# Performance work log

Measured on AMD Instinct MI355X. Metric: run time of the kernel, lower is better.

The kernel has to match this reference:

```python
import jax, jax.numpy as jnp
import numpy as np

N_NODES = 10000
N_EDGES = 160000
HID = 256
NBOND = 6
NATOM = 62
NLAYERS = 6


def _lin_init(key, fan_in, fan_out):
    # torch nn.Linear default: U(-1/sqrt(fan_in), 1/sqrt(fan_in))
    kw, kb = jax.random.split(key)
    bound = 1.0 / np.sqrt(fan_in)
    w = jax.random.uniform(kw, (fan_in, fan_out), jnp.float32, -bound, bound)
    b = jax.random.uniform(kb, (fan_out,), jnp.float32, -bound, bound)
    return w, b


def setup_inputs() -> dict:
    key = jax.random.key(0)
    ks = jax.random.split(key, 32)
    atom_features = jax.random.normal(ks[0], (N_NODES, NATOM), jnp.float32)
    edge_index = jax.random.randint(ks[1], (2, N_EDGES), 0, N_NODES, jnp.int64 if jax.config.jax_enable_x64 else jnp.int32)
    edge_features = jax.random.normal(ks[2], (N_EDGES, NBOND), jnp.float32)

    embed_w, embed_b = _lin_init(ks[3], NATOM, HID)

    msg_in = 2 * HID + NBOND  # 518
    mw1, mb1, mw2, mb2 = [], [], [], []
    uw1, ub1, uw2, ub2 = [], [], [], []
    for i in range(NLAYERS):
        k = jax.random.split(ks[4 + i], 4)
        w, b = _lin_init(k[0], msg_in, HID); mw1.append(w); mb1.append(b)
        w, b = _lin_init(k[1], HID, HID); mw2.append(w); mb2.append(b)
        w, b = _lin_init(k[2], 2 * HID, HID); uw1.append(w); ub1.append(b)
        w, b = _lin_init(k[3], HID, HID); uw2.append(w); ub2.append(b)

    r_w1, r_b1 = _lin_init(ks[20], HID, HID)
    r_w2, r_b2 = _lin_init(ks[21], HID, HID // 2)
    r_w3, r_b3 = _lin_init(ks[22], HID // 2, 1)

    return {
        "atom_features": atom_features,
        "edge_index": edge_index,
        "edge_features": edge_features,
        "embed_w": embed_w, "embed_b": embed_b,
        "msg_w1": jnp.stack(mw1), "msg_b1": jnp.stack(mb1),
        "msg_w2": jnp.stack(mw2), "msg_b2": jnp.stack(mb2),
        "upd_w1": jnp.stack(uw1), "upd_b1": jnp.stack(ub1),
        "upd_w2": jnp.stack(uw2), "upd_b2": jnp.stack(ub2),
        "r_w1": r_w1, "r_b1": r_b1,
        "r_w2": r_w2, "r_b2": r_b2,
        "r_w3": r_w3, "r_b3": r_b3,
    }


def _mlp2(x, w1, b1, w2, b2):
    return jnp.maximum(x @ w1 + b1, 0.0) @ w2 + b2


def reference(atom_features, edge_index, edge_features,
              embed_w, embed_b,
              msg_w1, msg_b1, msg_w2, msg_b2,
              upd_w1, upd_b1, upd_w2, upd_b2,
              r_w1, r_b1, r_w2, r_b2, r_w3, r_b3):
    src, dst = edge_index[0], edge_index[1]
    n = atom_features.shape[0]
    x = atom_features @ embed_w + embed_b  # [N, H]
    for l in range(msg_w1.shape[0]):
        # per-edge gather + concat -> message MLP
        msg_in = jnp.concatenate([x[src], x[dst], edge_features], axis=-1)  # [E, 2H+B]
        msgs = _mlp2(msg_in, msg_w1[l], msg_b1[l], msg_w2[l], msg_b2[l])  # [E, H]
        # scatter-add into dst nodes
        agg = jax.ops.segment_sum(msgs, dst, num_segments=n)  # [N, H]
        x = _mlp2(jnp.concatenate([x, agg], axis=-1), upd_w1[l], upd_b1[l], upd_w2[l], upd_b2[l])
    # readout (dropout is identity in eval mode)
    h = jnp.maximum(x @ r_w1 + r_b1, 0.0)
    h = jnp.maximum(h @ r_w2 + r_b2, 0.0)
    out = h @ r_w3 + r_b3  # [N, 1]
    return out.mean(axis=0)  # [1]
```

## Files before the change

### kernel.cpp

```cpp
#include <hip/hip_runtime.h>
#include <hip/hip_bf16.h>
#include <hip/hip_fp16.h>


#define HID 256

typedef _Float16 h8 __attribute__((ext_vector_type(8)));
typedef float f32x4 __attribute__((ext_vector_type(4)));

__device__ __forceinline__ void unpack_h8(const int4& r, float* f) {
    const __half2* h = reinterpret_cast<const __half2*>(&r);
#pragma unroll
    for (int k = 0; k < 4; ++k) {
        float2 t = __half22float2(h[k]);
        f[2 * k] = t.x;
        f[2 * k + 1] = t.y;
    }
}

__device__ __forceinline__ void unpack_h4(const int2& r, float* f) {
    const __half2* h = reinterpret_cast<const __half2*>(&r);
    float2 t0 = __half22float2(h[0]);
    float2 t1 = __half22float2(h[1]);
    f[0] = t0.x; f[1] = t0.y; f[2] = t1.x; f[3] = t1.y;
}

__device__ __forceinline__ void gld16(const void* g, void* l) {
    __builtin_amdgcn_global_load_lds(
        (const __attribute__((address_space(1))) void*)g,
        (__attribute__((address_space(3))) void*)l, 16, 0, 0);
}

__device__ __forceinline__ int swz(int row) { return (row + (row >> 2)) & 3; }


__global__ void hist_act_kernel(const int* __restrict__ dst, int* __restrict__ deg,
                                int E, const float* __restrict__ atom,
                                __half* __restrict__ atomH, int NA) {
    int i = blockIdx.x * blockDim.x + threadIdx.x;
    if (i < E) atomicAdd(&deg[dst[i]], 1);
    if (i < NA) {
        int r = i >> 3, seg = i & 7;
        h8 v;
#pragma unroll
        for (int j = 0; j < 8; ++j) {
            int c = seg * 8 + j;
            v[j] = (_Float16)((c < 62) ? atom[(size_t)r * 62 + c] : 0.f);
        }
        *reinterpret_cast<h8*>(&atomH[(size_t)r * 64 + seg * 8]) = v;
    }
}

__global__ __launch_bounds__(256) void scan_kernel(
    const int* __restrict__ deg, int* __restrict__ offs, float* __restrict__ degf, int n) {
    __shared__ int ws[4];
    const int t = threadIdx.x;
    const int lane = t & 63;
    const int w = t >> 6;
    const int per = (n + 255) / 256;
    const int s = t * per;
    const int e = min(s + per, n);
    int sum = 0;
    for (int i = s; i < e; ++i) sum += deg[i];
    int v = sum;
#pragma unroll
    for (int off = 1; off < 64; off <<= 1) {
        int u = __shfl_up(v, off, 64);
        if (lane >= off) v += u;
    }
    if (lane == 63) ws[w] = v;
    __syncthreads();
    if (t == 0) {
        int c = 0;
#pragma unroll
        for (int i = 0; i < 4; ++i) { int x = ws[i]; ws[i] = c; c += x; }
    }
    __syncthreads();
    int run = ws[w] + v - sum;
    for (int i = s; i < e; ++i) {
        int d = deg[i];
        offs[i] = run;
        degf[i] = (float)d;
        run += d;
    }
    if (e == n) offs[n] = run;
}


struct CDesc {
    const float* src;
    __half* dst;
    int Kreal, Kpad, srcN, tile0;
};
struct CTab {
    CDesc d[32];
    int nd;
};

__device__ void convert_body(const CTab& tab, int bid) {
    int idx = 0;
    for (int i = 1; i < tab.nd; ++i)
        if (tab.d[i].tile0 <= bid) idx = i;
    const CDesc d = tab.d[idx];
    const int q = bid - d.tile0;
    const int ntN = d.srcN >> 6;
    const int kb = (q / ntN) * 32;
    const int nb = (q % ntN) * 64;
    const int n = nb + (threadIdx.x & 63);
    const int k0 = kb + (threadIdx.x >> 6) * 8;
    h8 v;
#pragma unroll
    for (int j = 0; j < 8; ++j) {
        int k = k0 + j;
        v[j] = (_Float16)((k < d.Kreal) ? d.src[(size_t)k * d.srcN + n] : 0.f);
    }
    *reinterpret_cast<h8*>(&d.dst[(size_t)n * d.Kpad + k0]) = v;
}

__global__ __launch_bounds__(256) void scatter_conv_kernel(
    const int* __restrict__ src, const int* __restrict__ dst,
    const int* __restrict__ offs, int* __restrict__ cursor,
    int* __restrict__ csr_src, const float* __restrict__ ef,
    __half* __restrict__ ef8, int E, int sblocks, CTab tab) {
    if ((int)blockIdx.x < sblocks) {
        int i = blockIdx.x * blockDim.x + threadIdx.x;
        if (i < E) {
            int d = dst[i];
            int pos = atomicAdd(&cursor[d], 1);
            int idx = offs[d] + pos;
            csr_src[idx] = src[i];
            const float* s6 = ef + (size_t)i * 6;
            unsigned short h[8];
#pragma unroll
            for (int j = 0; j < 6; ++j) h[j] = __half_as_ushort(__float2half_rn(s6[j]));
            h[6] = 0; h[7] = 0;
            int4 pk;
            pk.x = (int)(h[0] | ((unsigned)h[1] << 16));
            pk.y = (int)(h[2] | ((unsigned)h[3] << 16));
            pk.z = (int)(h[4] | ((unsigned)h[5] << 16));
            pk.w = (int)(h[6] | ((unsigned)h[7] << 16));
            *reinterpret_cast<int4*>(ef8 + (size_t)idx * 8) = pk;
        }
    } else {
        convert_body(tab, blockIdx.x - sblocks);
    }
}


struct BDesc { float* out; const float* base; const float* v1; const float* B1;
               const float* v2; const float* B2; };
struct BTab { BDesc d[31]; };


#define ASTR 40

struct FDesc { const float* U2; const __half* Wfb; __half* dst; };
struct FTab { FDesc d[22]; };

__global__ __launch_bounds__(256) void fold_bias_kernel(FTab tab, BTab bt, int fblocks) {
    if ((int)blockIdx.x >= fblocks) {
        const BDesc d = bt.d[blockIdx.x - fblocks];
        const int j = threadIdx.x;
        float acc = d.base ? d.base[j] : 0.f;
        if (d.v1)
            for (int k = 0; k < 256; ++k) acc = fmaf(d.v1[k], d.B1[(size_t)k * 256 + j], acc);
        if (d.v2)
            for (int k = 0; k < 256; ++k) acc = fmaf(d.v2[k], d.B2[(size_t)k * 256 + j], acc);
        d.out[j] = acc;
        return;
    }
    const FDesc dd = tab.d[blockIdx.x >> 4];
    const int t4 = blockIdx.x & 15;
    const int rowBase = (t4 >> 2) * 64;
    const int colBase = (t4 & 3) * 64;

    __shared__ __align__(16) _Float16 Ah[64 * ASTR];
    __shared__ __align__(16) _Float16 Bh[64 * ASTR];

    const int tid = threadIdx.x;
    const int lane = tid & 63;
    const int wave = tid >> 6;
    const int waveM = (wave >> 1) * 32;
    const int waveN = (wave & 1) * 32;
    const int m0 = lane & 15;
    const int quad = lane >> 4;
    const int sr = tid >> 2;
    const int sseg = tid & 3;

    const f32x4 z = {0.f, 0.f, 0.f, 0.f};
    f32x4 acc[2][2] = {{z, z}, {z, z}};

    for (int kb = 0; kb < 256; kb += 32) {
        {
            size_t off = (size_t)(rowBase + sr) * 256 + kb + sseg * 8;
            *reinterpret_cast<int4*>(&Ah[sr * ASTR + sseg * 8]) =
                *reinterpret_cast<const int4*>(&dd.Wfb[off]);
        }
        {
            const float* Bp = dd.U2 + (size_t)(colBase + sr) * 256 + kb + sseg * 8;
            float4 u0 = *reinterpret_cast<const float4*>(Bp);
            float4 u1 = *reinterpret_cast<const float4*>(Bp + 4);
            h8 v;
            v[0] = (_Float16)u0.x; v[1] = (_Float16)u0.y;
            v[2] = (_Float16)u0.z; v[3] = (_Float16)u0.w;
            v[4] = (_Float16)u1.x; v[5] = (_Float16)u1.y;
            v[6] = (_Float16)u1.z; v[7] = (_Float16)u1.w;
            *reinterpret_cast<h8*>(&Bh[sr * ASTR + sseg * 8]) = v;
        }
        __syncthreads();

        const h8 a0 = *reinterpret_cast<const h8*>(&Ah[(waveM + m0) * ASTR + quad * 8]);
        const h8 a1 = *reinterpret_cast<const h8*>(&Ah[(waveM + 16 + m0) * ASTR + quad * 8]);
        const h8 b0 = *reinterpret_cast<const h8*>(&Bh[(waveN + m0) * ASTR + quad * 8]);
        const h8 b1 = *reinterpret_cast<const h8*>(&Bh[(waveN + 16 + m0) * ASTR + quad * 8]);

        acc[0][0] = __builtin_amdgcn_mfma_f32_16x16x32_f16(a0, b0, acc[0][0], 0, 0, 0);
        acc[0][1] = __builtin_amdgcn_mfma_f32_16x16x32_f16(a0, b1, acc[0][1], 0, 0, 0);
        acc[1][0] = __builtin_amdgcn_mfma_f32_16x16x32_f16(a1, b0, acc[1][0], 0, 0, 0);
        acc[1][1] = __builtin_amdgcn_mfma_f32_16x16x32_f16(a1, b1, acc[1][1], 0, 0, 0);

        __syncthreads();
    }

#pragma unroll
    for (int tm = 0; tm < 2; ++tm)
#pragma unroll
        for (int reg = 0; reg < 4; ++reg) {
            int n = rowBase + waveM + tm * 16 + quad * 4 + reg;
#pragma unroll
            for (int tn = 0; tn < 2; ++tn) {
                int k = colBase + waveN + tn * 16 + m0;
                dd.dst[(size_t)n * 256 + k] = __float2half_rn(acc[tm][tn][reg]);
            }
        }
}


template <int TN>
__global__ __launch_bounds__(256) void mfma_gemm(
    const __half* __restrict__ A, int lda,
    const __half* __restrict__ W, int K,
    const float* __restrict__ bias, const float* __restrict__ bias2,
    const float* __restrict__ rowscale,
    const __half* __restrict__ addend, int astride,
    __half* __restrict__ C, int M, int Nc, int do_relu) {
    constexpr int BUF = 4096 + TN * 2048;
    __shared__ __align__(16) unsigned char lds[2 * BUF];

    const int tid = threadIdx.x;
    const int lane = tid & 63;
    const int wave = tid >> 6;
    const int m0 = lane & 15;
    const int quad = lane >> 4;
    const int waveM = (wave >> 1) * 32;
    const int waveN = (wave & 1) * (TN * 16);
    const int rowBase = blockIdx.x * 64;
    const int colBase = blockIdx.y * (TN * 32);

    const int sa_r = tid >> 2;
    const int sa_ks = (tid & 3) ^ swz(sa_r);
    const int sa_row = min(rowBase + sa_r, M - 1);
    const int sb_r1 = sa_r + 64;
    const int sb_ks1 = (tid & 3) ^ swz(sb_r1);

    int aoff[2], boff[TN];
#pragma unroll
    for (int tm = 0; tm < 2; ++tm) {
        int r = waveM + tm * 16 + m0;
        aoff[tm] = ((r << 2) + (quad ^ swz(r))) << 4;
    }
#pragma unroll
    for (int tn = 0; tn < TN; ++tn) {
        int r = waveN + tn * 16 + m0;
        boff[tn] = 4096 + (((r << 2) + (quad ^ swz(r))) << 4);
    }

    const f32x4 z = {0.f, 0.f, 0.f, 0.f};
    f32x4 acc[2][TN];
#pragma unroll
    for (int tm = 0; tm < 2; ++tm)
#pragma unroll
        for (int tn = 0; tn < TN; ++tn) acc[tm][tn] = z;

    const __half* ga = A + (size_t)sa_row * lda + sa_ks * 8;
    const __half* gb0 = W + (size_t)(colBase + sa_r) * K + sa_ks * 8;
    const __half* gb1 = W + (size_t)(colBase + sb_r1) * K + sb_ks1 * 8;

    auto issue = [&](int p, int kb) {
        unsigned char* base = lds + p * BUF;
        gld16(ga + kb, base + wave * 1024);
        gld16(gb0 + kb, base + 4096 + wave * 1024);
        if constexpr (TN == 4) gld16(gb1 + kb, base + 8192 + wave * 1024);
    };

    issue(0, 0);
    int p = 0;
    for (int kb = 0; kb < K; kb += 32) {
        const bool has_next = (kb + 32 < K);
        if (has_next) issue(p ^ 1, kb + 32);
        if (has_next) {
            if constexpr (TN == 4)
                asm volatile("s_waitcnt vmcnt(3)" ::: "memory");
            else
                asm volatile("s_waitcnt vmcnt(2)" ::: "memory");
        } else {
            asm volatile("s_waitcnt vmcnt(0)" ::: "memory");
        }
        asm volatile("s_barrier" ::: "memory");

        const unsigned char* base = lds + p * BUF;
        h8 ah[2], bh[TN];
#pragma unroll
        for (int tm = 0; tm < 2; ++tm)
            ah[tm] = *reinterpret_cast<const h8*>(base + aoff[tm]);
#pragma unroll
        for (int tn = 0; tn < TN; ++tn)
            bh[tn] = *reinterpret_cast<const h8*>(base + boff[tn]);
#pragma unroll
        for (int tm = 0; tm < 2; ++tm)
#pragma unroll
            for (int tn = 0; tn < TN; ++tn)
                acc[tm][tn] = __builtin_amdgcn_mfma_f32_16x16x32_f16(
                    ah[tm], bh[tn], acc[tm][tn], 0, 0, 0);
        asm volatile("s_waitcnt lgkmcnt(0)" ::: "memory");
        asm volatile("s_barrier" ::: "memory");
        p ^= 1;
    }

    float cb[TN], db[TN];
    int col[TN];
#pragma unroll
    for (int tn = 0; tn < TN; ++tn) {
        col[tn] = colBase + waveN + tn * 16 + m0;
        cb[tn] = bias ? bias[col[tn]] : 0.f;
        db[tn] = bias2 ? bias2[col[tn]] : 0.f;
    }
#pragma unroll
    for (int tm = 0; tm < 2; ++tm) {
#pragma unroll
        for (int reg = 0; reg < 4; ++reg) {
            int row = rowBase + waveM + tm * 16 + quad * 4 + reg;
            if (row >= M) continue;
            float rs = rowscale ? rowscale[row] : 0.0f;
#pragma unroll
            for (int tn = 0; tn < TN; ++tn) {
                float v = acc[tm][tn][reg] + cb[tn] + rs * db[tn];
                if (addend)
                    v += __half2float(addend[(size_t)row * astride + col[tn]]);
                if (do_relu) v = fmaxf(v, 0.f);
                C[(size_t)row * Nc + col[tn]] = __float2half_rn(v);
            }
        }
    }
}


__global__ __launch_bounds__(256) void aggregate_kernel(
    const __half* __restrict__ PQ, const __half* __restrict__ ef8,
    const int* __restrict__ offs, const int* __restrict__ csr_src,
    const float* __restrict__ W1c, __half* __restrict__ Hagg, int n) {
    const int wave = threadIdx.x >> 6;
    const int lane = threadIdx.x & 63;
    const int node = blockIdx.x * 4 + wave;
    if (node >= n) return;
    const int ch = lane * 4;

    float wc[6][4];
#pragma unroll
    for (int k = 0; k < 6; ++k) {
        float4 w0 = *reinterpret_cast<const float4*>(W1c + k * HID + ch);
        wc[k][0] = w0.x; wc[k][1] = w0.y; wc[k][2] = w0.z; wc[k][3] = w0.w;
    }
    float qb[4];
    unpack_h4(*reinterpret_cast<const int2*>(PQ + (size_t)node * 768 + 256 + ch), qb);

    float acc[4] = {0.f, 0.f, 0.f, 0.f};

    auto fma_edge = [&](const int2& praw, const int4& eraw) {
        float p[4], e[8];
        unpack_h4(praw, p);
        unpack_h8(eraw, e);
#pragma unroll
        for (int i = 0; i < 4; ++i) {
            float h = p[i] + qb[i];
            h = fmaf(e[0], wc[0][i], h);
            h = fmaf(e[1], wc[1][i], h);
            h = fmaf(e[2], wc[2][i], h);
            h = fmaf(e[3], wc[3][i], h);
            h = fmaf(e[4], wc[4][i], h);
            h = fmaf(e[5], wc[5][i], h);
            acc[i] += fmaxf(h, 0.f);
        }
    };

    const int beg = offs[node];
    const int end = offs[node + 1];
    int j = beg;

    while (j + 6 <= end) {
        int s0 = csr_src[j];
        int s1 = csr_src[j + 1];
        int s2 = csr_src[j + 2];
        int s3 = csr_src[j + 3];
        int s4 = csr_src[j + 4];
        int s5 = csr_src[j + 5];
        int4 e0 = *reinterpret_cast<const int4*>(ef8 + (size_t)j * 8);
        int4 e1 = *reinterpret_cast<const int4*>(ef8 + (size_t)(j + 1) * 8);
        int4 e2 = *reinterpret_cast<const int4*>(ef8 + (size_t)(j + 2) * 8);
        int4 e3 = *reinterpret_cast<const int4*>(ef8 + (size_t)(j + 3) * 8);
        int4 e4 = *reinterpret_cast<const int4*>(ef8 + (size_t)(j + 4) * 8);
        int4 e5 = *reinterpret_cast<const int4*>(ef8 + (size_t)(j + 5) * 8);
        int2 p0 = *reinterpret_cast<const int2*>(PQ + (size_t)s0 * 768 + ch);
        int2 p1 = *reinterpret_cast<const int2*>(PQ + (size_t)s1 * 768 + ch);
        int2 p2 = *reinterpret_cast<const int2*>(PQ + (size_t)s2 * 768 + ch);
        int2 p3 = *reinterpret_cast<const int2*>(PQ + (size_t)s3 * 768 + ch);
        int2 p4 = *reinterpret_cast<const int2*>(PQ + (size_t)s4 * 768 + ch);
        int2 p5 = *reinterpret_cast<const int2*>(PQ + (size_t)s5 * 768 + ch);
        fma_edge(p0, e0);
        fma_edge(p1, e1);
        fma_edge(p2, e2);
        fma_edge(p3, e3);
        fma_edge(p4, e4);
        fma_edge(p5, e5);
        j += 6;
    }
    while (j + 2 <= end) {
        int s0 = csr_src[j];
        int s1 = csr_src[j + 1];
        int4 e0 = *reinterpret_cast<const int4*>(ef8 + (size_t)j * 8);
        int4 e1 = *reinterpret_cast<const int4*>(ef8 + (size_t)(j + 1) * 8);
        int2 p0 = *reinterpret_cast<const int2*>(PQ + (size_t)s0 * 768 + ch);
        int2 p1 = *reinterpret_cast<const int2*>(PQ + (size_t)s1 * 768 + ch);
        fma_edge(p0, e0);
        fma_edge(p1, e1);
        j += 2;
    }
    if (j < end) {
        int s = csr_src[j];
        int4 e = *reinterpret_cast<const int4*>(ef8 + (size_t)j * 8);
        int2 pw = *reinterpret_cast<const int2*>(PQ + (size_t)s * 768 + ch);
        fma_edge(pw, e);
    }

    unsigned short hs[4];
#pragma unroll
    for (int i = 0; i < 4; ++i) hs[i] = __half_as_ushort(__float2half_rn(acc[i]));
    int2 pk;
    pk.x = (int)(hs[0] | ((unsigned)hs[1] << 16));
    pk.y = (int)(hs[2] | ((unsigned)hs[3] << 16));
    *reinterpret_cast<int2*>(Hagg + (size_t)node * HID + ch) = pk;
}


__global__ __launch_bounds__(256) void readout_kernel(
    const __half* __restrict__ U5, const __half* __restrict__ wF,
    const float* __restrict__ cbF, const __half* __restrict__ wR2,
    const float* __restrict__ bR2, const float* __restrict__ w3,
    const float* __restrict__ b3, float* __restrict__ accum,
    int* __restrict__ done, float* __restrict__ outp, int M, int nblocks) {
    __shared__ __align__(16) unsigned char lds[24576 + 64 * 272 * 2];
    _Float16* h1 = (_Float16*)(lds + 24576);

    const int tid = threadIdx.x;
    const int lane = tid & 63;
    const int wave = tid >> 6;
    const int m0 = lane & 15;
    const int quad = lane >> 4;
    const int waveM = (wave >> 1) * 32;
    const int waveN = (wave & 1) * 64;
    const int rowBase = blockIdx.x * 64;

    const int sa_r = tid >> 2;
    const int sa_ks = (tid & 3) ^ swz(sa_r);
    const int sa_row = min(rowBase + sa_r, M - 1);
    const int sb_r1 = sa_r + 64;
    const int sb_ks1 = (tid & 3) ^ swz(sb_r1);

    int aoff[2], boff[4];
#pragma unroll
    for (int tm = 0; tm < 2; ++tm) {
        int r = waveM + tm * 16 + m0;
        aoff[tm] = ((r << 2) + (quad ^ swz(r))) << 4;
    }
#pragma unroll
    for (int tn = 0; tn < 4; ++tn) {
        int r = waveN + tn * 16 + m0;
        boff[tn] = (((r << 2) + (quad ^ swz(r))) << 4);
    }

    constexpr int BUF = 4096 + 4 * 2048;
    const f32x4 z = {0.f, 0.f, 0.f, 0.f};

    for (int half = 0; half < 2; ++half) {
        const __half* W = wF + (size_t)(half * 128) * 256;
        f32x4 acc[2][4] = {{z, z, z, z}, {z, z, z, z}};
        const __half* ga = U5 + (size_t)sa_row * 256 + sa_ks * 8;
        const __half* gb0 = W + (size_t)sa_r * 256 + sa_ks * 8;
        const __half* gb1 = W + (size_t)sb_r1 * 256 + sb_ks1 * 8;

        auto issue = [&](int p, int kb) {
            unsigned char* base = lds + p * BUF;
            gld16(ga + kb, base + wave * 1024);
            gld16(gb0 + kb, base + 4096 + wave * 1024);
            gld16(gb1 + kb, base + 8192 + wave * 1024);
        };
        issue(0, 0);
        int p = 0;
        for (int kb = 0; kb < 256; kb += 32) {
            const bool has_next = (kb + 32 < 256);
            if (has_next) issue(p ^ 1, kb + 32);
            if (has_next) asm volatile("s_waitcnt vmcnt(3)" ::: "memory");
            else asm volatile("s_waitcnt vmcnt(0)" ::: "memory");
            asm volatile("s_barrier" ::: "memory");
            const unsigned char* base = lds + p * BUF;
            h8 ah[2], bh[4];
#pragma unroll
            for (int tm = 0; tm < 2; ++tm)
                ah[tm] = *reinterpret_cast<const h8*>(base + aoff[tm]);
#pragma unroll
            for (int tn = 0; tn < 4; ++tn)
                bh[tn] = *reinterpret_cast<const h8*>(base + 4096 + boff[tn]);
#pragma unroll
            for (int tm = 0; tm < 2; ++tm)
#pragma unroll
                for (int tn = 0; tn < 4; ++tn)
                    acc[tm][tn] = __builtin_amdgcn_mfma_f32_16x16x32_f16(
                        ah[tm], bh[tn], acc[tm][tn], 0, 0, 0);
            asm volatile("s_waitcnt lgkmcnt(0)" ::: "memory");
            asm volatile("s_barrier" ::: "memory");
            p ^= 1;
        }
#pragma unroll
        for (int tm = 0; tm < 2; ++tm)
#pragma unroll
            for (int reg = 0; reg < 4; ++reg) {
                int r = waveM + tm * 16 + quad * 4 + reg;
#pragma unroll
                for (int tn = 0; tn < 4; ++tn) {
                    int c = half * 128 + waveN + tn * 16 + m0;
                    float v = acc[tm][tn][reg] + cbF[c];
                    h1[r * 272 + c] = (_Float16)fmaxf(v, 0.f);
                }
            }
        __syncthreads();
    }

    f32x4 acc2[2][4] = {{z, z, z, z}, {z, z, z, z}};
    auto issueB = [&](int p, int kb) {
        unsigned char* base = lds + p * 8192;
        gld16(wR2 + (size_t)sa_r * 256 + sa_ks * 8 + kb, base + wave * 1024);
        gld16(wR2 + (size_t)sb_r1 * 256 + sb_ks1 * 8 + kb, base + 4096 + wave * 1024);
    };
    issueB(0, 0);
    int p = 0;
    for (int kb = 0; kb < 256; kb += 32) {
        const bool has_next = (kb + 32 < 256);
        if (has_next) issueB(p ^ 1, kb + 32);
        if (has_next) asm volatile("s_waitcnt vmcnt(2)" ::: "memory");
        else asm volatile("s_waitcnt vmcnt(0)" ::: "memory");
        asm volatile("s_barrier" ::: "memory");
        const unsigned char* base = lds + p * 8192;
        h8 ah[2], bh[4];
#pragma unroll
        for (int tm = 0; tm < 2; ++tm)
            ah[tm] = *reinterpret_cast<const h8*>(
                &h1[(waveM + tm * 16 + m0) * 272 + kb + quad * 8]);
#pragma unroll
        for (int tn = 0; tn < 4; ++tn)
            bh[tn] = *reinterpret_cast<const h8*>(base + boff[tn]);
#pragma unroll
        for (int tm = 0; tm < 2; ++tm)
#pragma unroll
            for (int tn = 0; tn < 4; ++tn)
                acc2[tm][tn] = __builtin_amdgcn_mfma_f32_16x16x32_f16(
                    ah[tm], bh[tn], acc2[tm][tn], 0, 0, 0);
        asm volatile("s_waitcnt lgkmcnt(0)" ::: "memory");
        asm volatile("s_barrier" ::: "memory");
        p ^= 1;
    }

    float s = 0.f;
#pragma unroll
    for (int tm = 0; tm < 2; ++tm)
#pragma unroll
        for (int reg = 0; reg < 4; ++reg) {
            int row = rowBase + waveM + tm * 16 + quad * 4 + reg;
            if (row >= M) continue;
#pragma unroll
            for (int tn = 0; tn < 4; ++tn) {
                int c = waveN + tn * 16 + m0;
                float v = acc2[tm][tn][reg] + bR2[c];
                s += fmaxf(v, 0.f) * w3[c];
            }
        }
    __syncthreads();
    float* red = (float*)lds;
    red[tid] = s;
    __syncthreads();
    for (int off = 128; off > 0; off >>= 1) {
        if (tid < off) red[tid] += red[tid + off];
        __syncthreads();
    }
    if (tid == 0) {
        atomicAdd(accum, red[0]);
        __threadfence();
        int old = atomicAdd(done, 1);
        if (old == nblocks - 1) {
            float tot = atomicAdd(accum, 0.0f);
            outp[0] = tot / (float)M + b3[0];
        }
    }
}


extern "C" void kernel_launch(void* const* d_in, const int* in_sizes, int n_in,
                              void* d_out, int out_size, void* d_ws, size_t ws_size,
                              hipStream_t stream) {
    const float* atom   = (const float*)d_in[0];
    const int*   eidx   = (const int*)d_in[1];
    const float* ef     = (const float*)d_in[2];
    const float* emb_w  = (const float*)d_in[3];
    const float* emb_b  = (const float*)d_in[4];
    const float* msg_w1 = (const float*)d_in[5];
    const float* msg_b1 = (const float*)d_in[6];
    const float* msg_w2 = (const float*)d_in[7];
    const float* msg_b2 = (const float*)d_in[8];
    const float* upd_w1 = (const float*)d_in[9];
    const float* upd_b1 = (const float*)d_in[10];
    const float* upd_w2 = (const float*)d_in[11];
    const float* upd_b2 = (const float*)d_in[12];
    const float* r_w1   = (const float*)d_in[13];
    const float* r_b1   = (const float*)d_in[14];
    const float* r_w2   = (const float*)d_in[15];
    const float* r_b2   = (const float*)d_in[16];
    const float* r_w3   = (const float*)d_in[17];
    const float* r_b3   = (const float*)d_in[18];

    const int N = in_sizes[0] / 62;
    const int E = in_sizes[1] / 2;
    const int L = in_sizes[5] / (518 * 256);
    const int* src = eidx;
    const int* dst = eidx + E;

    char* wp = (char*)d_ws;
    auto alloc = [&](size_t bytes) -> void* {
        void* p = (void*)wp;
        wp += (bytes + 255) & ~(size_t)255;
        return p;
    };
    int*   deg     = (int*)alloc((size_t)N * 4);
    int*   cursor  = (int*)alloc((size_t)N * 4);
    float* accum   = (float*)alloc(256);
    int*   done    = (int*)((char*)accum + 16);
    size_t zero_bytes = (size_t)((char*)accum - (char*)d_ws) + 256;
    float* degf    = (float*)alloc((size_t)N * 4);
    int*   offs    = (int*)alloc((size_t)(N + 1) * 4);
    int*   csr_src = (int*)alloc((size_t)E * 4);
    __half* ef8    = (__half*)alloc((size_t)E * 8 * 2);

    const int SQ_P = 256 * 256;
    __half* w_emb = (__half*)alloc((size_t)256 * 64 * 2);
    __half* w_r2  = (__half*)alloc((size_t)128 * 256 * 2);
    __half* wF    = (__half*)alloc((size_t)SQ_P * 2);
    __half *wPQR[6], *wM3_[6];
    for (int l = 0; l < L; ++l) {
        wPQR[l] = (__half*)alloc((size_t)768 * 256 * 2);
        wM3_[l] = (__half*)alloc((size_t)SQ_P * 2);
    }
    __half* fb[22];
    for (int i = 0; i < 22; ++i) fb[i] = (__half*)alloc((size_t)SQ_P * 2);
    float* bvec = (float*)alloc((size_t)19 * 256 * 4);
    float* b768 = (float*)alloc((size_t)L * 768 * 4);

    __half* atomH = (__half*)alloc((size_t)N * 64 * 2);
    __half* bufX0 = (__half*)alloc((size_t)N * HID * 2);
    __half* bufX1 = (__half*)alloc((size_t)N * HID * 2);
    __half* PQR   = (__half*)alloc((size_t)N * 768 * 2);
    __half* HaggH = (__half*)alloc((size_t)N * HID * 2);

    hipMemsetAsync(d_ws, 0, zero_bytes, stream);

    const int hag = max(E, N * 8);
    hist_act_kernel<<<(hag + 255) / 256, 256, 0, stream>>>(dst, deg, E, atom, atomH, N * 8);
    scan_kernel<<<1, 256, 0, stream>>>(deg, offs, degf, N);

    CTab ct1;
    int nd = 0, tiles = 0;
    auto addDesc = [&](CTab& ct, const float* s, __half* dh, int Kreal, int Kpad,
                       int srcN) {
        ct.d[nd] = {s, dh, Kreal, Kpad, srcN, tiles};
        tiles += (Kpad / 32) * (srcN / 64);
        ++nd;
    };
    addDesc(ct1, emb_w, w_emb, 62, 64, 256);
    addDesc(ct1, msg_w1, wPQR[0], 256, 256, 256);
    addDesc(ct1, msg_w1 + 256 * 256, wPQR[0] + SQ_P, 256, 256, 256);
    addDesc(ct1, upd_w1, wPQR[0] + 2 * SQ_P, 256, 256, 256);
    addDesc(ct1, r_w2, w_r2, 256, 256, 128);
    for (int l = 1; l < L; ++l) {
        addDesc(ct1, msg_w1 + (size_t)l * 518 * 256,             fb[l - 1], 256, 256, 256);
        addDesc(ct1, msg_w1 + (size_t)l * 518 * 256 + 256 * 256, fb[4 + l], 256, 256, 256);
        addDesc(ct1, upd_w1 + (size_t)l * 512 * 256,             fb[9 + l], 256, 256, 256);
    }
    for (int l = 0; l < L; ++l)
        addDesc(ct1, upd_w1 + (size_t)l * 512 * 256 + 256 * 256, fb[15 + l], 256, 256, 256);
    addDesc(ct1, r_w1, fb[21], 256, 256, 256);
    ct1.nd = nd;

    const int sblocks = (E + 255) / 256;
    scatter_conv_kernel<<<sblocks + tiles, 256, 0, stream>>>(
        src, dst, offs, cursor, csr_src, ef, ef8, E, sblocks, ct1);

    FTab ft;
    for (int l = 1; l < L; ++l) {
        const float* U2p = upd_w2 + (size_t)(l - 1) * SQ_P;
        ft.d[l - 1] = {U2p, fb[l - 1], wPQR[l]};
        ft.d[4 + l] = {U2p, fb[4 + l], wPQR[l] + SQ_P};
        ft.d[9 + l] = {U2p, fb[9 + l], wPQR[l] + 2 * SQ_P};
    }
    for (int l = 0; l < L; ++l)
        ft.d[15 + l] = {msg_w2 + (size_t)l * SQ_P, fb[15 + l], wM3_[l]};
    ft.d[21] = {upd_w2 + (size_t)5 * SQ_P, fb[21], wF};

    BTab bt;
    int nb = 0;
    for (int l = 0; l < L; ++l) {
        const float* ub2p = (l > 0) ? upd_b2 + (size_t)(l - 1) * 256 : nullptr;
        bt.d[nb++] = {b768 + (size_t)l * 768 + 256, msg_b1 + (size_t)l * 256,
                      ub2p, msg_w1 + (size_t)l * 518 * 256,
                      ub2p, msg_w1 + (size_t)l * 518 * 256 + 256 * 256};
        bt.d[nb++] = {b768 + (size_t)l * 768, nullptr, nullptr, nullptr, nullptr, nullptr};
        bt.d[nb++] = {b768 + (size_t)l * 768 + 512, nullptr, nullptr, nullptr, nullptr, nullptr};
        bt.d[nb++] = {bvec + (size_t)(6 + l) * 256, upd_b1 + (size_t)l * 256,
                      ub2p, upd_w1 + (size_t)l * 512 * 256, nullptr, nullptr};
        bt.d[nb++] = {bvec + (size_t)(12 + l) * 256, nullptr,
                      msg_b2 + (size_t)l * 256, upd_w1 + (size_t)l * 512 * 256 + 256 * 256,
                      nullptr, nullptr};
    }
    bt.d[nb++] = {bvec + (size_t)18 * 256, r_b1, upd_b2 + (size_t)5 * 256, r_w1,
                  nullptr, nullptr};
    fold_bias_kernel<<<22 * 16 + nb, 256, 0, stream>>>(ft, bt, 22 * 16);

    const int mblk = (N + 63) / 64;
    dim3 blk(256);

    mfma_gemm<2><<<dim3(mblk, 4), blk, 0, stream>>>(
        atomH, 64, w_emb, 64,
        emb_b, nullptr, nullptr, nullptr, 0,
        bufX0, N, HID, 0);

    __half* U_prev = bufX0;
    __half* U_next = bufX1;
    for (int l = 0; l < L; ++l) {
        const float* w1c = msg_w1 + (size_t)l * 518 * 256 + 512 * 256;

        mfma_gemm<4><<<dim3(mblk, 6), blk, 0, stream>>>(
            U_prev, HID, wPQR[l], HID,
            b768 + (size_t)l * 768, nullptr, nullptr, nullptr, 0,
            PQR, N, 768, 0);
        aggregate_kernel<<<(N + 3) / 4, blk, 0, stream>>>(
            PQR, ef8, offs, csr_src, w1c, HaggH, N);
        mfma_gemm<2><<<dim3(mblk, 4), blk, 0, stream>>>(
            HaggH, HID, wM3_[l], HID,
            bvec + (size_t)(6 + l) * 256, bvec + (size_t)(12 + l) * 256, degf,
            PQR + 512, 768,
            U_next, N, HID, 1);
        __half* t = U_prev; U_prev = U_next; U_next = t;
    }

    readout_kernel<<<mblk, blk, 0, stream>>>(
        U_prev, wF, bvec + (size_t)18 * 256, w_r2, r_b2, r_w3, r_b3,
        accum, done, (float*)d_out, N, mblk);
}
```

Measured before the change: 478.6 us.

## Fold R projection into update GEMM via concatenated K, fuse embed into fold kernel

The third projection (R = U·Wr) is no longer computed in the PQR GEMM and re-read as an fp16 addend. Instead the update GEMM now takes K=512, loading its A operand from Hagg for the first half and from U_prev for the second, with the weights concatenated. This shrinks the PQ buffer from 768 to 512 columns and drops the addend read, and it keeps R in fp32 accumulation rather than rounding it to fp16. The embedding GEMM is also merged into the fold/bias launch as extra blocks, saving one kernel launch; the embed blocks do not depend on the fold outputs.

Measured after the change: 446.6 us. 6.7% less time.

```diff
diff --git a/kernel.cpp b/kernel.cpp
--- a/kernel.cpp
+++ b/kernel.cpp
@@ -90,7 +90,7 @@
 struct CDesc {
     const float* src;
     __half* dst;
-    int Kreal, Kpad, srcN, tile0;
+    int Kreal, Kpad, srcN, tile0, dstStride;
 };
 struct CTab {
     CDesc d[32];
@@ -114,7 +114,7 @@
         int k = k0 + j;
         v[j] = (_Float16)((k < d.Kreal) ? d.src[(size_t)k * d.srcN + n] : 0.f);
     }
-    *reinterpret_cast<h8*>(&d.dst[(size_t)n * d.Kpad + k0]) = v;
+    *reinterpret_cast<h8*>(&d.dst[(size_t)n * d.dstStride + k0]) = v;
 }
 
 __global__ __launch_bounds__(256) void scatter_conv_kernel(
@@ -154,28 +154,14 @@
 
 #define ASTR 40
 
-struct FDesc { const float* U2; const __half* Wfb; __half* dst; };
+struct FDesc { const float* U2; const __half* Wfb; __half* dst; int stride; };
 struct FTab { FDesc d[22]; };
 
-__global__ __launch_bounds__(256) void fold_bias_kernel(FTab tab, BTab bt, int fblocks) {
-    if ((int)blockIdx.x >= fblocks) {
-        const BDesc d = bt.d[blockIdx.x - fblocks];
-        const int j = threadIdx.x;
-        float acc = d.base ? d.base[j] : 0.f;
-        if (d.v1)
-            for (int k = 0; k < 256; ++k) acc = fmaf(d.v1[k], d.B1[(size_t)k * 256 + j], acc);
-        if (d.v2)
-            for (int k = 0; k < 256; ++k) acc = fmaf(d.v2[k], d.B2[(size_t)k * 256 + j], acc);
-        d.out[j] = acc;
-        return;
-    }
-    const FDesc dd = tab.d[blockIdx.x >> 4];
-    const int t4 = blockIdx.x & 15;
+__device__ void fold_tile(unsigned char* ldsraw, const FDesc& dd, int t4) {
+    _Float16* Ah = (_Float16*)ldsraw;
+    _Float16* Bh = (_Float16*)(ldsraw + 64 * ASTR * 2);
     const int rowBase = (t4 >> 2) * 64;
     const int colBase = (t4 & 3) * 64;
-
-    __shared__ __align__(16) _Float16 Ah[64 * ASTR];
-    __shared__ __align__(16) _Float16 Bh[64 * ASTR];
 
     const int tid = threadIdx.x;
     const int lane = tid & 63;
@@ -230,22 +216,21 @@
 #pragma unroll
             for (int tn = 0; tn < 2; ++tn) {
                 int k = colBase + waveN + tn * 16 + m0;
-                dd.dst[(size_t)n * 256 + k] = __float2half_rn(acc[tm][tn][reg]);
+                dd.dst[(size_t)n * dd.stride + k] = __float2half_rn(acc[tm][tn][reg]);
             }
         }
 }
 
 
 template <int TN>
-__global__ __launch_bounds__(256) void mfma_gemm(
-    const __half* __restrict__ A, int lda,
+__device__ void gemm_tile(
+    unsigned char* lds, int bx, int by,
+    const __half* __restrict__ A, int lda, const __half* __restrict__ A2,
     const __half* __restrict__ W, int K,
     const float* __restrict__ bias, const float* __restrict__ bias2,
     const float* __restrict__ rowscale,
-    const __half* __restrict__ addend, int astride,
     __half* __restrict__ C, int M, int Nc, int do_relu) {
     constexpr int BUF = 4096 + TN * 2048;
-    __shared__ __align__(16) unsigned char lds[2 * BUF];
 
     const int tid = threadIdx.x;
     const int lane = tid & 63;
@@ -254,8 +239,8 @@
     const int quad = lane >> 4;
     const int waveM = (wave >> 1) * 32;
     const int waveN = (wave & 1) * (TN * 16);
-    const int rowBase = blockIdx.x * 64;
-    const int colBase = blockIdx.y * (TN * 32);
+    const int rowBase = bx * 64;
+    const int colBase = by * (TN * 32);
 
     const int sa_r = tid >> 2;
     const int sa_ks = (tid & 3) ^ swz(sa_r);
@@ -283,12 +268,14 @@
         for (int tn = 0; tn < TN; ++tn) acc[tm][tn] = z;
 
     const __half* ga = A + (size_t)sa_row * lda + sa_ks * 8;
+    const __half* ga2 = A2 ? A2 + (size_t)sa_row * lda + sa_ks * 8 : nullptr;
     const __half* gb0 = W + (size_t)(colBase + sa_r) * K + sa_ks * 8;
     const __half* gb1 = W + (size_t)(colBase + sb_r1) * K + sb_ks1 * 8;
 
     auto issue = [&](int p, int kb) {
         unsigned char* base = lds + p * BUF;
-        gld16(ga + kb, base + wave * 1024);
+        const __half* as = (A2 && kb >= 256) ? (ga2 + (kb - 256)) : (ga + kb);
+        gld16(as, base + wave * 1024);
         gld16(gb0 + kb, base + 4096 + wave * 1024);
         if constexpr (TN == 4) gld16(gb1 + kb, base + 8192 + wave * 1024);
     };
@@ -345,13 +332,52 @@
 #pragma unroll
             for (int tn = 0; tn < TN; ++tn) {
                 float v = acc[tm][tn][reg] + cb[tn] + rs * db[tn];
-                if (addend)
-                    v += __half2float(addend[(size_t)row * astride + col[tn]]);
                 if (do_relu) v = fmaxf(v, 0.f);
                 C[(size_t)row * Nc + col[tn]] = __float2half_rn(v);
             }
         }
     }
+}
+
+template <int TN>
+__global__ __launch_bounds__(256) void mfma_gemm(
+    const __half* __restrict__ A, int lda, const __half* __restrict__ A2,
+    const __half* __restrict__ W, int K,
+    const float* __restrict__ bias, const float* __restrict__ bias2,
+    const float* __restrict__ rowscale,
+    __half* __restrict__ C, int M, int Nc, int do_relu) {
+    __shared__ __align__(16) unsigned char lds[2 * (4096 + TN * 2048)];
+    gemm_tile<TN>(lds, blockIdx.x, blockIdx.y, A, lda, A2, W, K,
+                  bias, bias2, rowscale, C, M, Nc, do_relu);
+}
+
+
+__global__ __launch_bounds__(256) void fold_bias_embed_kernel(
+    FTab ft, BTab bt, int fblocks, int bblocks,
+    const __half* __restrict__ atomH, const __half* __restrict__ w_emb,
+    const float* __restrict__ emb_b, __half* __restrict__ outX,
+    int M, int mblk) {
+    __shared__ __align__(16) unsigned char lds[16384];
+    int b = blockIdx.x;
+    if (b < fblocks) {
+        fold_tile(lds, ft.d[b >> 4], b & 15);
+        return;
+    }
+    b -= fblocks;
+    if (b < bblocks) {
+        const BDesc d = bt.d[b];
+        const int j = threadIdx.x;
+        float acc = d.base ? d.base[j] : 0.f;
+        if (d.v1)
+            for (int k = 0; k < 256; ++k) acc = fmaf(d.v1[k], d.B1[(size_t)k * 256 + j], acc);
+        if (d.v2)
+            for (int k = 0; k < 256; ++k) acc = fmaf(d.v2[k], d.B2[(size_t)k * 256 + j], acc);
+        d.out[j] = acc;
+        return;
+    }
+    b -= bblocks;
+    gemm_tile<2>(lds, b % mblk, b / mblk, atomH, 64, nullptr, w_emb, 64,
+                 emb_b, nullptr, nullptr, outX, M, HID, 0);
 }
 
 
@@ -372,7 +398,7 @@
         wc[k][0] = w0.x; wc[k][1] = w0.y; wc[k][2] = w0.z; wc[k][3] = w0.w;
     }
     float qb[4];
-    unpack_h4(*reinterpret_cast<const int2*>(PQ + (size_t)node * 768 + 256 + ch), qb);
+    unpack_h4(*reinterpret_cast<const int2*>(PQ + (size_t)node * 512 + 256 + ch), qb);
 
     float acc[4] = {0.f, 0.f, 0.f, 0.f};
 
@@ -410,12 +436,12 @@
         int4 e3 = *reinterpret_cast<const int4*>(ef8 + (size_t)(j + 3) * 8);
         int4 e4 = *reinterpret_cast<const int4*>(ef8 + (size_t)(j + 4) * 8);
         int4 e5 = *reinterpret_cast<const int4*>(ef8 + (size_t)(j + 5) * 8);
-        int2 p0 = *reinterpret_cast<const int2*>(PQ + (size_t)s0 * 768 + ch);
-        int2 p1 = *reinterpret_cast<const int2*>(PQ + (size_t)s1 * 768 + ch);
-        int2 p2 = *reinterpret_cast<const int2*>(PQ + (size_t)s2 * 768 + ch);
-        int2 p3 = *reinterpret_cast<const int2*>(PQ + (size_t)s3 * 768 + ch);
-        int2 p4 = *reinterpret_cast<const int2*>(PQ + (size_t)s4 * 768 + ch);
-        int2 p5 = *reinterpret_cast<const int2*>(PQ + (size_t)s5 * 768 + ch);
+        int2 p0 = *reinterpret_cast<const int2*>(PQ + (size_t)s0 * 512 + ch);
+        int2 p1 = *reinterpret_cast<const int2*>(PQ + (size_t)s1 * 512 + ch);
+        int2 p2 = *reinterpret_cast<const int2*>(PQ + (size_t)s2 * 512 + ch);
+        int2 p3 = *reinterpret_cast<const int2*>(PQ + (size_t)s3 * 512 + ch);
+        int2 p4 = *reinterpret_cast<const int2*>(PQ + (size_t)s4 * 512 + ch);
+        int2 p5 = *reinterpret_cast<const int2*>(PQ + (size_t)s5 * 512 + ch);
         fma_edge(p0, e0);
         fma_edge(p1, e1);
         fma_edge(p2, e2);
@@ -429,8 +455,8 @@
         int s1 = csr_src[j + 1];
         int4 e0 = *reinterpret_cast<const int4*>(ef8 + (size_t)j * 8);
         int4 e1 = *reinterpret_cast<const int4*>(ef8 + (size_t)(j + 1) * 8);
-        int2 p0 = *reinterpret_cast<const int2*>(PQ + (size_t)s0 * 768 + ch);
-        int2 p1 = *reinterpret_cast<const int2*>(PQ + (size_t)s1 * 768 + ch);
+        int2 p0 = *reinterpret_cast<const int2*>(PQ + (size_t)s0 * 512 + ch);
+        int2 p1 = *reinterpret_cast<const int2*>(PQ + (size_t)s1 * 512 + ch);
         fma_edge(p0, e0);
         fma_edge(p1, e1);
         j += 2;
@@ -438,7 +464,7 @@
     if (j < end) {
         int s = csr_src[j];
         int4 e = *reinterpret_cast<const int4*>(ef8 + (size_t)j * 8);
-        int2 pw = *reinterpret_cast<const int2*>(PQ + (size_t)s * 768 + ch);
+        int2 pw = *reinterpret_cast<const int2*>(PQ + (size_t)s * 512 + ch);
         fma_edge(pw, e);
     }
 
@@ -662,20 +688,20 @@
     __half* w_emb = (__half*)alloc((size_t)256 * 64 * 2);
     __half* w_r2  = (__half*)alloc((size_t)128 * 256 * 2);
     __half* wF    = (__half*)alloc((size_t)SQ_P * 2);
-    __half *wPQR[6], *wM3_[6];
+    __half *wPQ[6], *wUPD[6];
     for (int l = 0; l < L; ++l) {
-        wPQR[l] = (__half*)alloc((size_t)768 * 256 * 2);
-        wM3_[l] = (__half*)alloc((size_t)SQ_P * 2);
+        wPQ[l]  = (__half*)alloc((size_t)512 * 256 * 2);
+        wUPD[l] = (__half*)alloc((size_t)256 * 512 * 2);
     }
     __half* fb[22];
     for (int i = 0; i < 22; ++i) fb[i] = (__half*)alloc((size_t)SQ_P * 2);
     float* bvec = (float*)alloc((size_t)19 * 256 * 4);
-    float* b768 = (float*)alloc((size_t)L * 768 * 4);
+    float* b512 = (float*)alloc((size_t)L * 512 * 4);
 
     __half* atomH = (__half*)alloc((size_t)N * 64 * 2);
     __half* bufX0 = (__half*)alloc((size_t)N * HID * 2);
     __half* bufX1 = (__half*)alloc((size_t)N * HID * 2);
-    __half* PQR   = (__half*)alloc((size_t)N * 768 * 2);
+    __half* PQ    = (__half*)alloc((size_t)N * 512 * 2);
     __half* HaggH = (__half*)alloc((size_t)N * HID * 2);
 
     hipMemsetAsync(d_ws, 0, zero_bytes, stream);
@@ -686,25 +712,25 @@
 
     CTab ct1;
     int nd = 0, tiles = 0;
-    auto addDesc = [&](CTab& ct, const float* s, __half* dh, int Kreal, int Kpad,
-                       int srcN) {
-        ct.d[nd] = {s, dh, Kreal, Kpad, srcN, tiles};
+    auto addDesc = [&](const float* s, __half* dh, int Kreal, int Kpad, int srcN,
+                       int dstStride) {
+        ct1.d[nd] = {s, dh, Kreal, Kpad, srcN, tiles, dstStride};
         tiles += (Kpad / 32) * (srcN / 64);
         ++nd;
     };
-    addDesc(ct1, emb_w, w_emb, 62, 64, 256);
-    addDesc(ct1, msg_w1, wPQR[0], 256, 256, 256);
-    addDesc(ct1, msg_w1 + 256 * 256, wPQR[0] + SQ_P, 256, 256, 256);
-    addDesc(ct1, upd_w1, wPQR[0] + 2 * SQ_P, 256, 256, 256);
-    addDesc(ct1, r_w2, w_r2, 256, 256, 128);
+    addDesc(emb_w, w_emb, 62, 64, 256, 64);
+    addDesc(msg_w1, wPQ[0], 256, 256, 256, 256);
+    addDesc(msg_w1 + 256 * 256, wPQ[0] + SQ_P, 256, 256, 256, 256);
+    addDesc(upd_w1, wUPD[0] + 256, 256, 256, 256, 512);
+    addDesc(r_w2, w_r2, 256, 256, 128, 256);
     for (int l = 1; l < L; ++l) {
-        addDesc(ct1, msg_w1 + (size_t)l * 518 * 256,             fb[l - 1], 256, 256, 256);
-        addDesc(ct1, msg_w1 + (size_t)l * 518 * 256 + 256 * 256, fb[4 + l], 256, 256, 256);
-        addDesc(ct1, upd_w1 + (size_t)l * 512 * 256,             fb[9 + l], 256, 256, 256);
+        addDesc(msg_w1 + (size_t)l * 518 * 256,             fb[l - 1], 256, 256, 256, 256);
+        addDesc(msg_w1 + (size_t)l * 518 * 256 + 256 * 256, fb[4 + l], 256, 256, 256, 256);
+        addDesc(upd_w1 + (size_t)l * 512 * 256,             fb[9 + l], 256, 256, 256, 256);
     }
     for (int l = 0; l < L; ++l)
-        addDesc(ct1, upd_w1 + (size_t)l * 512 * 256 + 256 * 256, fb[15 + l], 256, 256, 256);
-    addDesc(ct1, r_w1, fb[21], 256, 256, 256);
+        addDesc(upd_w1 + (size_t)l * 512 * 256 + 256 * 256, fb[15 + l], 256, 256, 256, 256);
+    addDesc(r_w1, fb[21], 256, 256, 256, 256);
     ct1.nd = nd;
 
     const int sblocks = (E + 255) / 256;
@@ -714,23 +740,22 @@
     FTab ft;
     for (int l = 1; l < L; ++l) {
         const float* U2p = upd_w2 + (size_t)(l - 1) * SQ_P;
-        ft.d[l - 1] = {U2p, fb[l - 1], wPQR[l]};
-        ft.d[4 + l] = {U2p, fb[4 + l], wPQR[l] + SQ_P};
-        ft.d[9 + l] = {U2p, fb[9 + l], wPQR[l] + 2 * SQ_P};
+        ft.d[l - 1] = {U2p, fb[l - 1], wPQ[l], 256};
+        ft.d[4 + l] = {U2p, fb[4 + l], wPQ[l] + SQ_P, 256};
+        ft.d[9 + l] = {U2p, fb[9 + l], wUPD[l] + 256, 512};
     }
     for (int l = 0; l < L; ++l)
-        ft.d[15 + l] = {msg_w2 + (size_t)l * SQ_P, fb[15 + l], wM3_[l]};
-    ft.d[21] = {upd_w2 + (size_t)5 * SQ_P, fb[21], wF};
+        ft.d[15 + l] = {msg_w2 + (size_t)l * SQ_P, fb[15 + l], wUPD[l], 512};
+    ft.d[21] = {upd_w2 + (size_t)5 * SQ_P, fb[21], wF, 256};
 
     BTab bt;
     int nb = 0;
     for (int l = 0; l < L; ++l) {
         const float* ub2p = (l > 0) ? upd_b2 + (size_t)(l - 1) * 256 : nullptr;
-        bt.d[nb++] = {b768 + (size_t)l * 768 + 256, msg_b1 + (size_t)l * 256,
+        bt.d[nb++] = {b512 + (size_t)l * 512 + 256, msg_b1 + (size_t)l * 256,
                       ub2p, msg_w1 + (size_t)l * 518 * 256,
                       ub2p, msg_w1 + (size_t)l * 518 * 256 + 256 * 256};
-        bt.d[nb++] = {b768 + (size_t)l * 768, nullptr, nullptr, nullptr, nullptr, nullptr};
-        bt.d[nb++] = {b768 + (size_t)l * 768 + 512, nullptr, nullptr, nullptr, nullptr, nullptr};
+        bt.d[nb++] = {b512 + (size_t)l * 512, nullptr, nullptr, nullptr, nullptr, nullptr};
         bt.d[nb++] = {bvec + (size_t)(6 + l) * 256, upd_b1 + (size_t)l * 256,
                       ub2p, upd_w1 + (size_t)l * 512 * 256, nullptr, nullptr};
         bt.d[nb++] = {bvec + (size_t)(12 + l) * 256, nullptr,
@@ -739,31 +764,27 @@
     }
     bt.d[nb++] = {bvec + (size_t)18 * 256, r_b1, upd_b2 + (size_t)5 * 256, r_w1,
                   nullptr, nullptr};
-    fold_bias_kernel<<<22 * 16 + nb, 256, 0, stream>>>(ft, bt, 22 * 16);
 
     const int mblk = (N + 63) / 64;
+    const int fblocks = 22 * 16;
+    fold_bias_embed_kernel<<<fblocks + nb + mblk * 4, 256, 0, stream>>>(
+        ft, bt, fblocks, nb, atomH, w_emb, emb_b, bufX0, N, mblk);
+
     dim3 blk(256);
-
-    mfma_gemm<2><<<dim3(mblk, 4), blk, 0, stream>>>(
-        atomH, 64, w_emb, 64,
-        emb_b, nullptr, nullptr, nullptr, 0,
-        bufX0, N, HID, 0);
-
     __half* U_prev = bufX0;
     __half* U_next = bufX1;
     for (int l = 0; l < L; ++l) {
         const float* w1c = msg_w1 + (size_t)l * 518 * 256 + 512 * 256;
 
-        mfma_gemm<4><<<dim3(mblk, 6), blk, 0, stream>>>(
-            U_prev, HID, wPQR[l], HID,
-            b768 + (size_t)l * 768, nullptr, nullptr, nullptr, 0,
-            PQR, N, 768, 0);
+        mfma_gemm<4><<<dim3(mblk, 4), blk, 0, stream>>>(
+            U_prev, HID, nullptr, wPQ[l], HID,
+            b512 + (size_t)l * 512, nullptr, nullptr,
+            PQ, N, 512, 0);
         aggregate_kernel<<<(N + 3) / 4, blk, 0, stream>>>(
-            PQR, ef8, offs, csr_src, w1c, HaggH, N);
+            PQ, ef8, offs, csr_src, w1c, HaggH, N);
         mfma_gemm<2><<<dim3(mblk, 4), blk, 0, stream>>>(
-            HaggH, HID, wM3_[l], HID,
+            HaggH, HID, U_prev, wUPD[l], 512,
             bvec + (size_t)(6 + l) * 256, bvec + (size_t)(12 + l) * 256, degf,
-            PQR + 512, 768,
             U_next, N, HID, 1);
         __half* t = U_prev; U_prev = U_next; U_next = t;
     }
```
